# Kernel tuning notes

Measured on AMD Instinct MI355X. Metric: run time of the kernel, lower is better.

## Reference

```python
import jax, jax.numpy as jnp
import numpy as np

EPS = 1e-6
BETA = 0.5
B, T, N = 128, 30, 10000   # batch, BP iterations, n error bits
M, K = 5000, 10            # checks, observables
CHK_W, OBS_W = 6, 50       # row weights of chkmat / obsmat


def _make_supports():
    """Deterministic sparse supports (CSR-style flattened col indices + row ids)."""
    rng = np.random.default_rng(0)
    chk_rows = np.argpartition(rng.random((M, N)), CHK_W, axis=1)[:, :CHK_W]
    obs_rows = np.argpartition(rng.random((K, N)), OBS_W, axis=1)[:, :OBS_W]
    chk_idx = chk_rows.reshape(-1).astype(np.int32)
    chk_seg = np.repeat(np.arange(M, dtype=np.int32), CHK_W)
    obs_idx = obs_rows.reshape(-1).astype(np.int32)
    obs_seg = np.repeat(np.arange(K, dtype=np.int32), OBS_W)
    return chk_idx, chk_seg, obs_idx, obs_seg


def setup_inputs() -> dict:
    key = jax.random.key(0)
    k1, k2, k3 = jax.random.split(key, 3)
    all_llrs = jax.random.normal(k1, (B, T, N), dtype=jnp.float32) * 2.0
    syndromes = jax.random.randint(k2, (B, M), 0, 2, dtype=jnp.int32)
    observables = jax.random.randint(k3, (B, K), 0, 2, dtype=jnp.int32)
    chk_idx, chk_seg, obs_idx, obs_seg = _make_supports()
    return {
        "all_llrs": all_llrs,
        "syndromes": syndromes,
        "observables": observables,
        "chk_idx": jnp.asarray(chk_idx),
        "chk_seg": jnp.asarray(chk_seg),
        "obs_idx": jnp.asarray(obs_idx),
        "obs_seg": jnp.asarray(obs_seg),
    }


def _pred_llr(t, idx, seg, num_seg):
    # t: (B,T,N) tanh(llr/2); gather support cols -> (B,T,E)
    g = t[:, :, idx]
    # segmented product over support entries (tanh rule), segments on axis 0
    p = jax.ops.segment_prod(jnp.moveaxis(g, 2, 0), seg, num_segments=num_seg)  # (S,B,T)
    p = jnp.clip(jnp.moveaxis(p, 0, 2), -1.0 + EPS, 1.0 - EPS)  # (B,T,S)
    return 2.0 * jnp.arctanh(p)


def _bce_with_logits(z, y):
    # stable BCEWithLogits: max(z,0) - z*y + log(1+exp(-|z|)) == logaddexp(0,z) - z*y
    return jnp.logaddexp(0.0, z) - z * y


def reference(all_llrs, syndromes, observables, chk_idx, chk_seg, obs_idx, obs_seg):
    t = jnp.tanh(all_llrs * 0.5)                                   # (B,T,N)
    syn_llr = _pred_llr(t, chk_idx, chk_seg, syndromes.shape[1])    # (B,T,M)
    obs_llr = _pred_llr(t, obs_idx, obs_seg, observables.shape[1])  # (B,T,K)
    y_syn = syndromes.astype(jnp.float32)[:, None, :]
    y_obs = observables.astype(jnp.float32)[:, None, :]
    loss1 = _bce_with_logits(-syn_llr, y_syn).sum(axis=2)           # (B,T)
    loss2 = _bce_with_logits(-obs_llr, y_obs).sum(axis=2)           # (B,T)
    loss = BETA * loss1 + (1.0 - BETA) * loss2
    return loss.mean()
```

## Files before the change

### kernel.cpp

```cpp
#include <hip/hip_runtime.h>

typedef float floatx2 __attribute__((ext_vector_type(2)));

#define B_  128
#define T_  30
#define N_  10000
#define M_  5000
#define K_  10
#define OBS_W_ 50
#define EPS_ 1e-6f
#define LOG2F_ 0.69314718056f
#define BT_  3840
#define CHUNK_ 100
#define NCHK_ (M_/CHUNK_)
#define NB_ 10

__global__ __launch_bounds__(256) void tanh_transpose_fp8(
    const float*   __restrict__ llrs,
    unsigned char* __restrict__ tt)
{
    __shared__ float tile[64][65];
    const int bt0 = blockIdx.x * 64;
    const int n0  = blockIdx.y * 64;
    const int tid = threadIdx.x;

    #pragma unroll
    for (int i = 0; i < 4; ++i) {
        int lin = i * 256 + tid;
        int r   = lin >> 4;
        int c4  = (lin & 15) * 4;
        if (n0 + c4 < N_) {
            float4 v = *(const float4*)(llrs + (size_t)(bt0 + r) * N_ + n0 + c4);
            tile[r][c4 + 0] = 1.f - 2.f / (__expf(v.x) + 1.f);
            tile[r][c4 + 1] = 1.f - 2.f / (__expf(v.y) + 1.f);
            tile[r][c4 + 2] = 1.f - 2.f / (__expf(v.z) + 1.f);
            tile[r][c4 + 3] = 1.f - 2.f / (__expf(v.w) + 1.f);
        }
    }
    __syncthreads();

    const int q  = tid & 15;
    const int cg = tid >> 4;
    #pragma unroll
    for (int i = 0; i < 4; ++i) {
        int col = cg + 16 * i;
        if (n0 + col < N_) {
            float v0 = tile[4 * q + 0][col];
            float v1 = tile[4 * q + 1][col];
            float v2 = tile[4 * q + 2][col];
            float v3 = tile[4 * q + 3][col];
            int pk = __builtin_amdgcn_cvt_pk_fp8_f32(v0, v1, 0, false);
            pk     = __builtin_amdgcn_cvt_pk_fp8_f32(v2, v3, pk, true);
            *(int*)(tt + (size_t)(n0 + col) * BT_ + bt0 + 4 * q) = pk;
        }
    }
}

__device__ __forceinline__ void cvt4(unsigned int qv, float* a) {
    floatx2 lo = __builtin_amdgcn_cvt_pk_f32_fp8((int)qv, false);
    floatx2 hi = __builtin_amdgcn_cvt_pk_f32_fp8((int)qv, true);
    a[0] = lo.x; a[1] = lo.y; a[2] = hi.x; a[3] = hi.y;
}

__global__ __launch_bounds__(256) void gather_loss_fp8(
    const unsigned char* __restrict__ tt,
    const int*           __restrict__ syndromes,
    const int*           __restrict__ observables,
    const int*           __restrict__ chk_idx,
    const int*           __restrict__ obs_idx,
    float*               __restrict__ out)
{
    __shared__ int   sidx[CHUNK_ * 6];
    __shared__ int   ssyn[NB_][CHUNK_];
    __shared__ float red[4];

    const int tid  = threadIdx.x;
    const int lane = tid & 63;
    const int wave = tid >> 6;
    const int r0   = blockIdx.x * 256 + lane * 4;
    const int bA   = r0 / 30;
    const int bB   = (r0 + 3) / 30;
    const int split= (bA + 1) * 30 - r0;
    const int b_lo = (blockIdx.x * 256) / 30;
    const unsigned char* col0 = tt + r0;
    const int y = blockIdx.y;
    float acc = 0.f;

    if (y < NCHK_) {
        const int m0 = y * CHUNK_;
        for (int i = tid; i < CHUNK_ * 6; i += 256)
            sidx[i] = chk_idx[m0 * 6 + i];
        for (int i = tid; i < NB_ * CHUNK_; i += 256) {
            int bi = i / CHUNK_, j = i - bi * CHUNK_;
            int b  = b_lo + bi; if (b > B_ - 1) b = B_ - 1;
            ((int*)ssyn)[i] = syndromes[(size_t)b * M_ + m0 + j];
        }
        __syncthreads();
        const int iA = bA - b_lo, iB = bB - b_lo;

        #pragma unroll 2
        for (int s = wave * 25; s < wave * 25 + 25; ++s) {
            int i0 = sidx[s * 6 + 0], i1 = sidx[s * 6 + 1], i2 = sidx[s * 6 + 2];
            int i3 = sidx[s * 6 + 3], i4 = sidx[s * 6 + 4], i5 = sidx[s * 6 + 5];
            unsigned int q0 = *(const unsigned int*)(col0 + (size_t)i0 * BT_);
            unsigned int q1 = *(const unsigned int*)(col0 + (size_t)i1 * BT_);
            unsigned int q2 = *(const unsigned int*)(col0 + (size_t)i2 * BT_);
            unsigned int q3 = *(const unsigned int*)(col0 + (size_t)i3 * BT_);
            unsigned int q4 = *(const unsigned int*)(col0 + (size_t)i4 * BT_);
            unsigned int q5 = *(const unsigned int*)(col0 + (size_t)i5 * BT_);
            float a[4], b4[4], p[4];
            cvt4(q0, p);  cvt4(q1, a);  cvt4(q2, b4);
            #pragma unroll
            for (int j = 0; j < 4; ++j) p[j] *= a[j] * b4[j];
            cvt4(q3, a);  cvt4(q4, b4);
            #pragma unroll
            for (int j = 0; j < 4; ++j) p[j] *= a[j] * b4[j];
            cvt4(q5, a);
            float sgA = ssyn[iA][s] ? -1.f : 1.f;
            float sgB = ssyn[iB][s] ? -1.f : 1.f;
            #pragma unroll
            for (int j = 0; j < 4; ++j) {
                float sg = (j >= split) ? sgB : sgA;
                float sp = sg * p[j] * a[j];
                sp = fminf(fmaxf(sp, -1.f + EPS_), 1.f - EPS_);
                acc += LOG2F_ - __logf(1.f + sp);
            }
        }
    } else {
        for (int k = wave; k < K_; k += 4) {
            const int* oi = obs_idx + k * OBS_W_;
            float p[4] = {1.f, 1.f, 1.f, 1.f};
            #pragma unroll 5
            for (int j2 = 0; j2 < OBS_W_; ++j2) {
                unsigned int qq = *(const unsigned int*)(col0 + (size_t)oi[j2] * BT_);
                float a[4];
                cvt4(qq, a);
                p[0] *= a[0]; p[1] *= a[1]; p[2] *= a[2]; p[3] *= a[3];
            }
            float sgA = observables[(size_t)bA * K_ + k] ? -1.f : 1.f;
            float sgB = observables[(size_t)bB * K_ + k] ? -1.f : 1.f;
            #pragma unroll
            for (int j = 0; j < 4; ++j) {
                float sg = (j >= split) ? sgB : sgA;
                float sp = sg * p[j];
                sp = fminf(fmaxf(sp, -1.f + EPS_), 1.f - EPS_);
                acc += LOG2F_ - __logf(1.f + sp);
            }
        }
    }

    #pragma unroll
    for (int off = 32; off > 0; off >>= 1)
        acc += __shfl_down(acc, off, 64);
    if (lane == 0) red[wave] = acc;
    __syncthreads();
    if (tid == 0) {
        float s = red[0] + red[1] + red[2] + red[3];
        atomicAdd(out, s * (0.5f / (float)BT_));
    }
}

extern "C" void kernel_launch(void* const* d_in, const int* in_sizes, int n_in,
                              void* d_out, int out_size, void* d_ws, size_t ws_size,
                              hipStream_t stream) {
    const float* all_llrs    = (const float*)d_in[0];
    const int*   syndromes   = (const int*)d_in[1];
    const int*   observables = (const int*)d_in[2];
    const int*   chk_idx     = (const int*)d_in[3];
    const int*   obs_idx     = (const int*)d_in[5];
    float*         out = (float*)d_out;
    unsigned char* tt  = (unsigned char*)d_ws;

    hipMemsetAsync(out, 0, sizeof(float) * out_size, stream);

    dim3 g1(BT_ / 64, (N_ + 63) / 64);
    tanh_transpose_fp8<<<g1, 256, 0, stream>>>(all_llrs, tt);

    dim3 g2(BT_ / 256, NCHK_ + 1);
    gather_loss_fp8<<<g2, 256, 0, stream>>>(
        tt, syndromes, observables, chk_idx, obs_idx, out);
}
```

Before: 275.4 us.

## Pack fp8 in registers before LDS transpose; shrink check chunks; read syndromes directly

The transpose kernel now computes tanh for a 4x4 sub-block in registers and packs it to fp8 before the LDS stage. The LDS tile therefore holds packed ints, and each thread writes 16 contiguous bytes instead of scattered 4-byte stores. The gather kernel uses chunks of 20 checks instead of 100, giving about five times more blocks along y, and fully unrolls 5 checks per wave. Syndromes are now read straight from global memory per thread rather than staged in shared memory, trading a staging loop and barrier cost for redundant scattered global loads.

```diff
diff --git a/kernel.cpp b/kernel.cpp
--- a/kernel.cpp
+++ b/kernel.cpp
@@ -11,48 +11,45 @@
 #define EPS_ 1e-6f
 #define LOG2F_ 0.69314718056f
 #define BT_  3840
-#define CHUNK_ 100
+#define CHUNK_ 20
 #define NCHK_ (M_/CHUNK_)
-#define NB_ 10
 
 __global__ __launch_bounds__(256) void tanh_transpose_fp8(
     const float*   __restrict__ llrs,
     unsigned char* __restrict__ tt)
 {
-    __shared__ float tile[64][65];
+    __shared__ unsigned int lds[64][20];
     const int bt0 = blockIdx.x * 64;
     const int n0  = blockIdx.y * 64;
     const int tid = threadIdx.x;
+    const int q   = tid & 15;
+    const int cg  = tid >> 4;
 
-    #pragma unroll
-    for (int i = 0; i < 4; ++i) {
-        int lin = i * 256 + tid;
-        int r   = lin >> 4;
-        int c4  = (lin & 15) * 4;
-        if (n0 + c4 < N_) {
-            float4 v = *(const float4*)(llrs + (size_t)(bt0 + r) * N_ + n0 + c4);
-            tile[r][c4 + 0] = 1.f - 2.f / (__expf(v.x) + 1.f);
-            tile[r][c4 + 1] = 1.f - 2.f / (__expf(v.y) + 1.f);
-            tile[r][c4 + 2] = 1.f - 2.f / (__expf(v.z) + 1.f);
-            tile[r][c4 + 3] = 1.f - 2.f / (__expf(v.w) + 1.f);
+    if (n0 + 4 * cg < N_) {
+        float t[4][4];
+        #pragma unroll
+        for (int j = 0; j < 4; ++j) {
+            float4 v = *(const float4*)(llrs +
+                        (size_t)(bt0 + 4 * q + j) * N_ + n0 + 4 * cg);
+            t[j][0] = 1.f - 2.f / (__expf(v.x) + 1.f);
+            t[j][1] = 1.f - 2.f / (__expf(v.y) + 1.f);
+            t[j][2] = 1.f - 2.f / (__expf(v.z) + 1.f);
+            t[j][3] = 1.f - 2.f / (__expf(v.w) + 1.f);
+        }
+        #pragma unroll
+        for (int k = 0; k < 4; ++k) {
+            int pk = __builtin_amdgcn_cvt_pk_fp8_f32(t[0][k], t[1][k], 0, false);
+            pk     = __builtin_amdgcn_cvt_pk_fp8_f32(t[2][k], t[3][k], pk, true);
+            lds[4 * cg + k][q] = (unsigned int)pk;
         }
     }
     __syncthreads();
 
-    const int q  = tid & 15;
-    const int cg = tid >> 4;
-    #pragma unroll
-    for (int i = 0; i < 4; ++i) {
-        int col = cg + 16 * i;
-        if (n0 + col < N_) {
-            float v0 = tile[4 * q + 0][col];
-            float v1 = tile[4 * q + 1][col];
-            float v2 = tile[4 * q + 2][col];
-            float v3 = tile[4 * q + 3][col];
-            int pk = __builtin_amdgcn_cvt_pk_fp8_f32(v0, v1, 0, false);
-            pk     = __builtin_amdgcn_cvt_pk_fp8_f32(v2, v3, pk, true);
-            *(int*)(tt + (size_t)(n0 + col) * BT_ + bt0 + 4 * q) = pk;
-        }
+    const int u = tid >> 6;
+    const int c = tid & 63;
+    if (n0 + c < N_) {
+        uint4 d = *(const uint4*)&lds[c][4 * u];
+        *(uint4*)(tt + (size_t)(n0 + c) * BT_ + bt0 + 16 * u) = d;
     }
 }
 
@@ -71,7 +68,6 @@
     float*               __restrict__ out)
 {
     __shared__ int   sidx[CHUNK_ * 6];
-    __shared__ int   ssyn[NB_][CHUNK_];
     __shared__ float red[4];
 
     const int tid  = threadIdx.x;
@@ -81,33 +77,28 @@
     const int bA   = r0 / 30;
     const int bB   = (r0 + 3) / 30;
     const int split= (bA + 1) * 30 - r0;
-    const int b_lo = (blockIdx.x * 256) / 30;
     const unsigned char* col0 = tt + r0;
     const int y = blockIdx.y;
     float acc = 0.f;
 
     if (y < NCHK_) {
         const int m0 = y * CHUNK_;
-        for (int i = tid; i < CHUNK_ * 6; i += 256)
-            sidx[i] = chk_idx[m0 * 6 + i];
-        for (int i = tid; i < NB_ * CHUNK_; i += 256) {
-            int bi = i / CHUNK_, j = i - bi * CHUNK_;
-            int b  = b_lo + bi; if (b > B_ - 1) b = B_ - 1;
-            ((int*)ssyn)[i] = syndromes[(size_t)b * M_ + m0 + j];
-        }
+        if (tid < CHUNK_ * 6) sidx[tid] = chk_idx[m0 * 6 + tid];
         __syncthreads();
-        const int iA = bA - b_lo, iB = bB - b_lo;
 
-        #pragma unroll 2
-        for (int s = wave * 25; s < wave * 25 + 25; ++s) {
-            int i0 = sidx[s * 6 + 0], i1 = sidx[s * 6 + 1], i2 = sidx[s * 6 + 2];
-            int i3 = sidx[s * 6 + 3], i4 = sidx[s * 6 + 4], i5 = sidx[s * 6 + 5];
-            unsigned int q0 = *(const unsigned int*)(col0 + (size_t)i0 * BT_);
-            unsigned int q1 = *(const unsigned int*)(col0 + (size_t)i1 * BT_);
-            unsigned int q2 = *(const unsigned int*)(col0 + (size_t)i2 * BT_);
-            unsigned int q3 = *(const unsigned int*)(col0 + (size_t)i3 * BT_);
-            unsigned int q4 = *(const unsigned int*)(col0 + (size_t)i4 * BT_);
-            unsigned int q5 = *(const unsigned int*)(col0 + (size_t)i5 * BT_);
+        const int mb = wave * 5;
+        #pragma unroll
+        for (int s = 0; s < 5; ++s) {
+            const int m  = m0 + mb + s;
+            const int* si = &sidx[(mb + s) * 6];
+            unsigned int q0 = *(const unsigned int*)(col0 + (size_t)si[0] * BT_);
+            unsigned int q1 = *(const unsigned int*)(col0 + (size_t)si[1] * BT_);
+            unsigned int q2 = *(const unsigned int*)(col0 + (size_t)si[2] * BT_);
+            unsigned int q3 = *(const unsigned int*)(col0 + (size_t)si[3] * BT_);
+            unsigned int q4 = *(const unsigned int*)(col0 + (size_t)si[4] * BT_);
+            unsigned int q5 = *(const unsigned int*)(col0 + (size_t)si[5] * BT_);
+            int synA = syndromes[(size_t)bA * M_ + m];
+            int synB = syndromes[(size_t)bB * M_ + m];
             float a[4], b4[4], p[4];
             cvt4(q0, p);  cvt4(q1, a);  cvt4(q2, b4);
             #pragma unroll
@@ -116,8 +107,8 @@
             #pragma unroll
             for (int j = 0; j < 4; ++j) p[j] *= a[j] * b4[j];
             cvt4(q5, a);
-            float sgA = ssyn[iA][s] ? -1.f : 1.f;
-            float sgB = ssyn[iB][s] ? -1.f : 1.f;
+            const float sgA = synA ? -1.f : 1.f;
+            const float sgB = synB ? -1.f : 1.f;
             #pragma unroll
             for (int j = 0; j < 4; ++j) {
                 float sg = (j >= split) ? sgB : sgA;
```

Result: slower. 317.2 us (+15.2%).
